# Kernel tuning notes

Measured on AMD Instinct MI355X. Metric: run time of the kernel, lower is better.

## Reference

```python
import jax, jax.numpy as jnp
import numpy as np

NEG_SLOPE = 0.2  # PyG GATConv default negative_slope
NUM_GRAPHS = 64
N, E, F_IN = 50000, 800000, 128


def _gat(x, src, dst, W, a_s, a_d, b, concat):
    # PyG GATConv: h = x W (per head); e_ij = leaky_relu(a_s.h_j + a_d.h_i);
    # softmax over incoming edges of each dst node; out_i = sum_j alpha_ij h_j
    n = x.shape[0]
    H, C = a_s.shape
    h = (x @ W).reshape(n, H, C)                     # [N,H,C]
    es = jnp.einsum('nhc,hc->nh', h, a_s)            # [N,H]
    ed = jnp.einsum('nhc,hc->nh', h, a_d)
    e = jax.nn.leaky_relu(es[src] + ed[dst], NEG_SLOPE)   # [E,H]
    m = jax.ops.segment_max(e, dst, num_segments=n)       # per-dst max (stable softmax)
    ex = jnp.exp(e - m[dst])
    den = jax.ops.segment_sum(ex, dst, num_segments=n)
    alpha = ex / den[dst]                                 # [E,H]
    out = jax.ops.segment_sum(h[src] * alpha[:, :, None], dst, num_segments=n)  # [N,H,C]
    if concat:
        return out.reshape(n, H * C) + b
    return out.mean(axis=1) + b


def setup_inputs() -> dict:
    key = jax.random.key(0)
    ks = jax.random.split(key, 10)
    x = jax.random.normal(ks[0], (N, F_IN), jnp.float32)
    edge_index = jax.random.randint(ks[1], (2, E), 0, N, dtype=jnp.int64)
    batch = jnp.sort(jax.random.randint(ks[2], (N,), 0, NUM_GRAPHS, dtype=jnp.int64))
    s1 = 1.0 / np.sqrt(F_IN)
    s2 = 1.0 / np.sqrt(256)
    return {
        'x': x,
        'edge_index': edge_index,
        'batch': batch,
        'W1': jax.random.normal(ks[3], (F_IN, 256), jnp.float32) * s1,
        'a_src1': jax.random.normal(ks[4], (4, 64), jnp.float32) * s2,
        'a_dst1': jax.random.normal(ks[5], (4, 64), jnp.float32) * s2,
        'b1': jnp.zeros((256,), jnp.float32),
        'W2': jax.random.normal(ks[6], (256, 128), jnp.float32) * s2,
        'a_src2': jax.random.normal(ks[7], (1, 128), jnp.float32) * (1.0 / np.sqrt(128)),
        'a_dst2': jax.random.normal(ks[8], (1, 128), jnp.float32) * (1.0 / np.sqrt(128)),
        'b2': jnp.zeros((128,), jnp.float32),
        'fc_w': jax.random.normal(ks[9], (128, 10), jnp.float32) * (1.0 / np.sqrt(128)),
        'fc_b': jnp.zeros((10,), jnp.float32),
    }


def reference(x, edge_index, batch, W1, a_src1, a_dst1, b1, W2, a_src2, a_dst2, b2, fc_w, fc_b):
    n = x.shape[0]
    loop = jnp.arange(n, dtype=edge_index.dtype)  # PyG add_self_loops=True
    src = jnp.concatenate([edge_index[0], loop])
    dst = jnp.concatenate([edge_index[1], loop])
    h = jax.nn.elu(_gat(x, src, dst, W1, a_src1, a_dst1, b1, True))   # dropout: eval mode -> identity
    h = jax.nn.elu(_gat(h, src, dst, W2, a_src2, a_dst2, b2, False))
    pooled = jax.ops.segment_sum(h, batch, num_segments=NUM_GRAPHS)
    cnt = jax.ops.segment_sum(jnp.ones((n,), h.dtype), batch, num_segments=NUM_GRAPHS)
    pooled = pooled / jnp.maximum(cnt, 1.0)[:, None]
    logits = pooled @ fc_w + fc_b
    return jax.nn.log_softmax(logits, axis=1)
```

## Files before the change

kernel.cpp:

```cpp
#include <hip/hip_runtime.h>
#include <math.h>

#define N_NODES 50000
#define N_PAD   50048
#define N_EDGES 800000
#define E_TOT   (N_EDGES + N_NODES)
#define NG 64
#define POOL_CHUNK 64
#define CAP 48
#define GEMM1_BLOCKS 3128
#define FILL_BLOCKS  3321
#define PH1_INTERLEAVE (2 * GEMM1_BLOCKS)
#define PH1_TOTAL (GEMM1_BLOCKS + FILL_BLOCKS)

typedef short short8 __attribute__((ext_vector_type(8)));
typedef float floatx4 __attribute__((ext_vector_type(4)));
typedef float floatx2 __attribute__((ext_vector_type(2)));

__device__ inline short f2bf(float f) {
    union { float f; unsigned u; } v; v.f = f;
    unsigned r = v.u + 0x7fff + ((v.u >> 16) & 1);
    return (short)(r >> 16);
}
__device__ inline float bf2f(short s) {
    union { float f; unsigned u; } v;
    v.u = ((unsigned)(unsigned short)s) << 16;
    return v.f;
}

__device__ inline unsigned f2fp8(float f) {
    union { float f; unsigned u; } v; v.f = f;
    unsigned s = v.u & 0x80000000u;
    unsigned au = v.u & 0x7fffffffu;
    if (au > 0x43E00000u) au = 0x43E00000u;
    unsigned r = au + 0x7ffffu + ((au >> 20) & 1);
    int e8 = (int)(r >> 23) - 120;
    unsigned m3 = (r >> 20) & 7;
    unsigned code;
    if (e8 <= 0) code = 0;
    else if (e8 > 15) code = 0x7e;
    else code = ((unsigned)e8 << 3) | m3;
    return (s >> 24) | code;
}

__device__ inline float leaky_exp(float t) {
    t = t > 0.f ? t : 0.2f * t;
    return __expf(t);
}


__global__ __launch_bounds__(256) void phase1_kernel(const float* __restrict__ x,
                                                     const float* __restrict__ W1,
                                                     const float* __restrict__ a_s,
                                                     const float* __restrict__ a_d,
                                                     const int* __restrict__ ei,
                                                     int* __restrict__ deg,
                                                     unsigned short* __restrict__ col,
                                                     unsigned char* __restrict__ C8,
                                                     float* __restrict__ es,
                                                     float* __restrict__ ed,
                                                     const float* __restrict__ W2,
                                                     const float* __restrict__ as2,
                                                     const float* __restrict__ ad2,
                                                     float* __restrict__ ws2,
                                                     float* __restrict__ wd2) {
    __shared__ short bs[64][136];
    int bid = blockIdx.x;
    int tid = threadIdx.x;

    if (bid == PH1_TOTAL) {
        int k = tid;
        float s = 0.f, d = 0.f;
        for (int c = 0; c < 128; c++) {
            float w = W2[k * 128 + c];
            s += w * as2[c];
            d += w * ad2[c];
        }
        ws2[k] = s;
        wd2[k] = d;
        return;
    }

    int gb, fb;
    if (bid < PH1_INTERLEAVE) {
        if (bid & 1) { fb = bid >> 1; gb = -1; }
        else         { gb = bid >> 1; fb = -1; }
    } else {
        fb = bid - GEMM1_BLOCKS; gb = -1;
    }

    if (fb >= 0) {
        int t = fb * 256 + tid;
        int s, d;
        if (t < N_EDGES) {
            s = ei[t];
            d = ei[N_EDGES + t];
        } else if (t < E_TOT) {
            s = d = t - N_EDGES;
        } else {
            return;
        }
        int slot = atomicAdd(&deg[d], 1);
        if (slot < CAP) col[d * CAP + slot] = (unsigned short)s;
        return;
    }

    const int K = 128, N = 256;
    int head = gb & 3;
    int bx = gb >> 2;
    int c0 = head * 64;

    int tc = tid & 63;
    int tk0 = (tid >> 6) * 32;
    for (int k = tk0; k < tk0 + 32; k++)
        bs[tc][k] = f2bf(W1[k * 256 + c0 + tc]);
    __syncthreads();

    int wid = tid >> 6;
    int lane = tid & 63;
    int m0 = bx * 64 + wid * 16;
    int mr = lane & 15;
    int quad = lane >> 4;
    int kq = quad << 3;
    int arow = m0 + mr; if (arow > N_NODES - 1) arow = N_NODES - 1;
    const float* aptr = x + (size_t)arow * K + kq;
    floatx4 acc[4] = {{0.f,0.f,0.f,0.f},{0.f,0.f,0.f,0.f},{0.f,0.f,0.f,0.f},{0.f,0.f,0.f,0.f}};
    for (int k0 = 0; k0 < K; k0 += 32) {
        float4 f0 = *(const float4*)(aptr + k0);
        float4 f1 = *(const float4*)(aptr + k0 + 4);
        short8 a;
        a[0] = f2bf(f0.x); a[1] = f2bf(f0.y); a[2] = f2bf(f0.z); a[3] = f2bf(f0.w);
        a[4] = f2bf(f1.x); a[5] = f2bf(f1.y); a[6] = f2bf(f1.z); a[7] = f2bf(f1.w);
#pragma unroll
        for (int t = 0; t < 4; t++) {
            short8 b = *(const short8*)&bs[t * 16 + mr][kq + k0];
            acc[t] = __builtin_amdgcn_mfma_f32_16x16x32_bf16(a, b, acc[t], 0, 0, 0);
        }
    }
    float asv[4], adv[4];
#pragma unroll
    for (int t = 0; t < 4; t++) {
        asv[t] = a_s[c0 + t * 16 + mr];
        adv[t] = a_d[c0 + t * 16 + mr];
    }
    int orow = m0 + (quad << 2);
#pragma unroll
    for (int r = 0; r < 4; r++) {
        float ps = acc[0][r] * asv[0] + acc[1][r] * asv[1] + acc[2][r] * asv[2] + acc[3][r] * asv[3];
        float pd = acc[0][r] * adv[0] + acc[1][r] * adv[1] + acc[2][r] * adv[2] + acc[3][r] * adv[3];
#pragma unroll
        for (int off = 8; off >= 1; off >>= 1) {
            ps += __shfl_xor(ps, off);
            pd += __shfl_xor(pd, off);
        }
        if (mr == 0) {
            es[(orow + r) * 4 + head] = ps;
            ed[(orow + r) * 4 + head] = pd;
        }
    }
#pragma unroll
    for (int t = 0; t < 4; t++) {
        int ocol = c0 + t * 16 + mr;
#pragma unroll
        for (int r = 0; r < 4; r++) {
            C8[(size_t)(orow + r) * N + ocol] = (unsigned char)f2fp8(acc[t][r]);
        }
    }
}


__global__ __launch_bounds__(256) void gather1_kernel(const unsigned char* __restrict__ h8,
                                                      const int* __restrict__ deg,
                                                      const unsigned short* __restrict__ col,
                                                      const float* __restrict__ es,
                                                      const float* __restrict__ ed,
                                                      const float* __restrict__ bias,
                                                      const float* __restrict__ ws2,
                                                      const float* __restrict__ wd2,
                                                      short* __restrict__ out,
                                                      float* __restrict__ es2,
                                                      float* __restrict__ ed2) {
    __shared__ float wlds[4][CAP * 4];
    int tid = threadIdx.x;
    int wid = tid >> 6;
    int n = __builtin_amdgcn_readfirstlane(blockIdx.x * 4 + wid);
    int l = tid & 63;
    int hh = l >> 4;
    int cnt = deg[n]; cnt = cnt < CAP ? cnt : CAP;
    int cnt8 = (cnt + 7) & ~7;

    {
        int eA = l >> 2;
        int hA = l & 3;
        float edvA = ed[n * 4 + hA];
#pragma unroll
        for (int p = 0; p < 3; p++) {
            int e = p * 16 + eA;
            if (e < cnt8) {
                int s = col[n * CAP + e];
                float w = (e < cnt) ? leaky_exp(es[s * 4 + hA] + edvA) : 0.f;
                wlds[wid][e * 4 + hA] = w;
            }
        }
    }

    const unsigned int* cp = (const unsigned int*)(col + n * CAP);
    float ax = 0.f, ay = 0.f, az = 0.f, aw = 0.f, den = 0.f;
    for (int eb = 0; eb < cnt8; eb += 8) {
        unsigned int cw0 = cp[(eb >> 1) + 0];
        unsigned int cw1 = cp[(eb >> 1) + 1];
        unsigned int cw2 = cp[(eb >> 1) + 2];
        unsigned int cw3 = cp[(eb >> 1) + 3];
        int idx[8];
        idx[0] = cw0 & 0xffff; idx[1] = cw0 >> 16;
        idx[2] = cw1 & 0xffff; idx[3] = cw1 >> 16;
        idx[4] = cw2 & 0xffff; idx[5] = cw2 >> 16;
        idx[6] = cw3 & 0xffff; idx[7] = cw3 >> 16;
        float wv[8];
#pragma unroll
        for (int j = 0; j < 8; j++) wv[j] = wlds[wid][(eb + j) * 4 + hh];
        unsigned hv[8];
#pragma unroll
        for (int j = 0; j < 8; j++)
            hv[j] = *(const unsigned*)&h8[(size_t)idx[j] * 256 + l * 4];
#pragma unroll
        for (int j = 0; j < 8; j++) {
            floatx2 lo = __builtin_amdgcn_cvt_pk_f32_fp8(hv[j], false);
            floatx2 hi = __builtin_amdgcn_cvt_pk_f32_fp8(hv[j], true);
            den += wv[j];
            ax += wv[j] * lo[0];
            ay += wv[j] * lo[1];
            az += wv[j] * hi[0];
            aw += wv[j] * hi[1];
        }
    }
    float inv = 1.0f / den;
    float4 bb = *(const float4*)&bias[l * 4];
    float o0 = ax * inv + bb.x;
    float o1 = ay * inv + bb.y;
    float o2 = az * inv + bb.z;
    float o3 = aw * inv + bb.w;
    o0 = o0 > 0.f ? o0 : __expf(o0) - 1.f;
    o1 = o1 > 0.f ? o1 : __expf(o1) - 1.f;
    o2 = o2 > 0.f ? o2 : __expf(o2) - 1.f;
    o3 = o3 > 0.f ? o3 : __expf(o3) - 1.f;
    short4 ob;
    ob.x = f2bf(o0); ob.y = f2bf(o1); ob.z = f2bf(o2); ob.w = f2bf(o3);
    *(short4*)&out[(size_t)n * 256 + l * 4] = ob;

    float4 s4 = *(const float4*)&ws2[l * 4];
    float4 d4 = *(const float4*)&wd2[l * 4];
    float ps = o0 * s4.x + o1 * s4.y + o2 * s4.z + o3 * s4.w;
    float pd = o0 * d4.x + o1 * d4.y + o2 * d4.z + o3 * d4.w;
#pragma unroll
    for (int off = 32; off >= 1; off >>= 1) {
        ps += __shfl_xor(ps, off);
        pd += __shfl_xor(pd, off);
    }
    if (l == 0) {
        es2[n] = ps;
        ed2[n] = pd;
    }
}


__global__ __launch_bounds__(256) void gemm2_kernel(const short* __restrict__ A,
                                                    const float* __restrict__ W2,
                                                    unsigned char* __restrict__ C8) {
    __shared__ short bs[64][264];
    const int K = 256, N = 128;
    int tid = threadIdx.x;
    int by = blockIdx.y;
    int c0 = by * 64;

    int tc = tid & 63;
    int tk0 = (tid >> 6) * 64;
    for (int k = tk0; k < tk0 + 64; k++)
        bs[tc][k] = f2bf(W2[k * 128 + c0 + tc]);
    __syncthreads();

    int wid = tid >> 6;
    int lane = tid & 63;
    int m0 = blockIdx.x * 64 + wid * 16;
    int mr = lane & 15;
    int quad = lane >> 4;
    int kq = quad << 3;
    const short* arow = A + (size_t)(m0 + mr) * K + kq;
    floatx4 acc[4] = {{0.f,0.f,0.f,0.f},{0.f,0.f,0.f,0.f},{0.f,0.f,0.f,0.f},{0.f,0.f,0.f,0.f}};
    for (int k0 = 0; k0 < K; k0 += 32) {
        short8 a = *(const short8*)(arow + k0);
#pragma unroll
        for (int t = 0; t < 4; t++) {
            short8 b = *(const short8*)&bs[t * 16 + mr][kq + k0];
            acc[t] = __builtin_amdgcn_mfma_f32_16x16x32_bf16(a, b, acc[t], 0, 0, 0);
        }
    }
    int orow = m0 + (quad << 2);
#pragma unroll
    for (int t = 0; t < 4; t++) {
        int ocol = c0 + t * 16 + mr;
#pragma unroll
        for (int r = 0; r < 4; r++) {
            C8[(size_t)(orow + r) * N + ocol] = (unsigned char)f2fp8(acc[t][r]);
        }
    }
}


__global__ __launch_bounds__(256) void gather2_kernel(const unsigned char* __restrict__ h8,
                                                      const int* __restrict__ deg,
                                                      const unsigned short* __restrict__ col,
                                                      const float* __restrict__ es2,
                                                      const float* __restrict__ ed2,
                                                      const float* __restrict__ bias,
                                                      short* __restrict__ out) {
    __shared__ float wlds[4][CAP];
    int tid = threadIdx.x;
    int wid = tid >> 6;
    int n = __builtin_amdgcn_readfirstlane(blockIdx.x * 4 + wid);
    int l = tid & 63;
    int cnt = deg[n]; cnt = cnt < CAP ? cnt : CAP;
    int cnt8 = (cnt + 7) & ~7;

    {
        float edv = ed2[n];
        if (l < cnt8) {
            int s = col[n * CAP + l];
            float w = (l < cnt) ? leaky_exp(es2[s] + edv) : 0.f;
            wlds[wid][l] = w;
        }
    }

    const unsigned int* cp = (const unsigned int*)(col + n * CAP);
    float ax = 0.f, ay = 0.f, den = 0.f;
    for (int eb = 0; eb < cnt8; eb += 8) {
        unsigned int cw0 = cp[(eb >> 1) + 0];
        unsigned int cw1 = cp[(eb >> 1) + 1];
        unsigned int cw2 = cp[(eb >> 1) + 2];
        unsigned int cw3 = cp[(eb >> 1) + 3];
        int idx[8];
        idx[0] = cw0 & 0xffff; idx[1] = cw0 >> 16;
        idx[2] = cw1 & 0xffff; idx[3] = cw1 >> 16;
        idx[4] = cw2 & 0xffff; idx[5] = cw2 >> 16;
        idx[6] = cw3 & 0xffff; idx[7] = cw3 >> 16;
        float wv[8];
#pragma unroll
        for (int j = 0; j < 8; j++) wv[j] = wlds[wid][eb + j];
        unsigned hv[8];
#pragma unroll
        for (int j = 0; j < 8; j++)
            hv[j] = *(const unsigned short*)&h8[(size_t)idx[j] * 128 + l * 2];
#pragma unroll
        for (int j = 0; j < 8; j++) {
            floatx2 lo = __builtin_amdgcn_cvt_pk_f32_fp8(hv[j], false);
            den += wv[j];
            ax += wv[j] * lo[0];
            ay += wv[j] * lo[1];
        }
    }
    float inv = 1.0f / den;
    float2 bb = *(const float2*)&bias[l * 2];
    float o0 = ax * inv + bb.x;
    float o1 = ay * inv + bb.y;
    o0 = o0 > 0.f ? o0 : __expf(o0) - 1.f;
    o1 = o1 > 0.f ? o1 : __expf(o1) - 1.f;
    short2 ob;
    ob.x = f2bf(o0); ob.y = f2bf(o1);
    *(short2*)&out[(size_t)n * 128 + l * 2] = ob;
}


__global__ __launch_bounds__(128) void pool1_kernel(const short* __restrict__ h,
                                                    const int* __restrict__ batch,
                                                    float* __restrict__ pooled) {
    int c = threadIdx.x;
    int n0 = blockIdx.x * POOL_CHUNK;
    int n1 = n0 + POOL_CHUNK;
    if (n1 > N_NODES) n1 = N_NODES;
    if (n0 >= n1) return;
    float acc = 0.f;
    int g = batch[n0];
    for (int n = n0; n < n1; n++) {
        int bg = batch[n];
        if (bg != g) {
            atomicAdd(&pooled[g * 128 + c], acc);
            acc = 0.f;
            g = bg;
        }
        acc += bf2f(h[n * 128 + c]);
    }
    atomicAdd(&pooled[g * 128 + c], acc);
}


__global__ void fc_kernel(const float* __restrict__ pooled, const int* __restrict__ batch,
                          const float* __restrict__ fcw, const float* __restrict__ fcb,
                          float* __restrict__ out) {
    int g = threadIdx.x;
    if (g >= NG) return;
    int lo = 0, hi = N_NODES;
    while (lo < hi) {
        int mid = (lo + hi) >> 1;
        if (batch[mid] < g) lo = mid + 1; else hi = mid;
    }
    int start = lo;
    lo = start; hi = N_NODES;
    while (lo < hi) {
        int mid = (lo + hi) >> 1;
        if (batch[mid] <= g) lo = mid + 1; else hi = mid;
    }
    int cnt = lo - start;
    float inv = 1.0f / (float)(cnt > 0 ? cnt : 1);

    float lg[10];
#pragma unroll
    for (int j = 0; j < 10; j++) lg[j] = fcb[j];
    for (int k = 0; k < 128; k++) {
        float p = pooled[g * 128 + k] * inv;
#pragma unroll
        for (int j = 0; j < 10; j++) lg[j] += p * fcw[k * 10 + j];
    }
    float m = lg[0];
#pragma unroll
    for (int j = 1; j < 10; j++) m = fmaxf(m, lg[j]);
    float se = 0.f;
#pragma unroll
    for (int j = 0; j < 10; j++) se += __expf(lg[j] - m);
    float lse = m + __logf(se);
#pragma unroll
    for (int j = 0; j < 10; j++) out[g * 10 + j] = lg[j] - lse;
}


extern "C" void kernel_launch(void* const* d_in, const int* in_sizes, int n_in,
                              void* d_out, int out_size, void* d_ws, size_t ws_size,
                              hipStream_t stream) {
    const float* x     = (const float*)d_in[0];
    const int*   ei    = (const int*)d_in[1];
    const int*   batch = (const int*)d_in[2];
    const float* W1    = (const float*)d_in[3];
    const float* as1   = (const float*)d_in[4];
    const float* ad1   = (const float*)d_in[5];
    const float* b1    = (const float*)d_in[6];
    const float* W2    = (const float*)d_in[7];
    const float* as2   = (const float*)d_in[8];
    const float* ad2   = (const float*)d_in[9];
    const float* b2    = (const float*)d_in[10];
    const float* fcw   = (const float*)d_in[11];
    const float* fcb   = (const float*)d_in[12];
    float* out = (float*)d_out;

    char* ws = (char*)d_ws;
    size_t off = 0;
    auto alloc = [&](size_t bytes) -> void* {
        void* p = ws + off;
        off = (off + bytes + 255) & ~(size_t)255;
        return p;
    };
    int* deg             = (int*)alloc(N_NODES * 4);
    float* pooled        = (float*)alloc(NG * 128 * 4);
    unsigned short* col  = (unsigned short*)alloc((size_t)N_NODES * CAP * 2);
    float* es1           = (float*)alloc((size_t)N_PAD * 4 * 4);
    float* ed1           = (float*)alloc((size_t)N_PAD * 4 * 4);
    float* es2           = (float*)alloc((size_t)N_PAD * 4);
    float* ed2           = (float*)alloc((size_t)N_PAD * 4);
    float* ws2           = (float*)alloc(256 * 4);
    float* wd2           = (float*)alloc(256 * 4);
    unsigned char* h1    = (unsigned char*)alloc((size_t)N_PAD * 256);
    short* h1p           = (short*)alloc((size_t)N_PAD * 256 * 2);
    unsigned char* h2    = (unsigned char*)alloc((size_t)N_PAD * 128);
    short* h2p           = (short*)alloc((size_t)N_PAD * 128 * 2);

    size_t zbytes = 200192 + ((size_t)NG * 128 * 4) + (size_t)N_NODES * CAP * 2;
    hipMemsetAsync(deg, 0, zbytes, stream);

    int ngrid = N_NODES / 4;

    phase1_kernel<<<PH1_TOTAL + 1, 256, 0, stream>>>(x, W1, as1, ad1, ei, deg, col, h1, es1, ed1,
                                                     W2, as2, ad2, ws2, wd2);
    gather1_kernel<<<ngrid, 256, 0, stream>>>(h1, deg, col, es1, ed1, b1, ws2, wd2,
                                              h1p, es2, ed2);
    gemm2_kernel<<<dim3(N_PAD / 64, 2), 256, 0, stream>>>(h1p, W2, h2);
    gather2_kernel<<<ngrid, 256, 0, stream>>>(h2, deg, col, es2, ed2, b2, h2p);

    pool1_kernel<<<(N_NODES + POOL_CHUNK - 1) / POOL_CHUNK, 128, 0, stream>>>(h2p, batch, pooled);
    fc_kernel<<<1, 64, 0, stream>>>(pooled, batch, fcw, fcb, out);
}
```

Measured before the change: 252.0 us.

## Shard CSR degree counters across 8 sub-buckets and compact adjacency in gather1

The edge-fill pass now spreads the per-destination atomic counters and adjacency slots across 8 shards chosen by block ID. This is meant to reduce atomic contention on the same deg entry and spread the col writes. gather1 merges the shards into a compact per-node list held in LDS, then writes a consolidated col/degT for gather2 to reuse. Block role interleaving between GEMM and fill blocks is also changed. The cost is more zeroing, 8 extra degree loads per node in gather1, and per-shard caps of 18 that could drop edges for skewed degrees.

```diff
diff --git a/kernel.cpp b/kernel.cpp
--- a/kernel.cpp
+++ b/kernel.cpp
@@ -8,6 +8,8 @@
 #define NG 64
 #define POOL_CHUNK 64
 #define CAP 48
+#define NSH 8
+#define SCAP 18
 #define GEMM1_BLOCKS 3128
 #define FILL_BLOCKS  3321
 #define PH1_INTERLEAVE (2 * GEMM1_BLOCKS)
@@ -54,8 +56,8 @@
                                                      const float* __restrict__ a_s,
                                                      const float* __restrict__ a_d,
                                                      const int* __restrict__ ei,
-                                                     int* __restrict__ deg,
-                                                     unsigned short* __restrict__ col,
+                                                     int* __restrict__ deg_s,
+                                                     unsigned short* __restrict__ col_s,
                                                      unsigned char* __restrict__ C8,
                                                      float* __restrict__ es,
                                                      float* __restrict__ ed,
@@ -81,12 +83,13 @@
         return;
     }
 
-    int gb, fb;
+    int gb = -1, fb = -1;
     if (bid < PH1_INTERLEAVE) {
-        if (bid & 1) { fb = bid >> 1; gb = -1; }
-        else         { gb = bid >> 1; fb = -1; }
+        int role = (bid ^ (bid >> 3)) & 1;
+        int gi = (bid >> 3) * 4 + ((bid & 7) >> 1);
+        if (role == 0) gb = gi; else fb = gi;
     } else {
-        fb = bid - GEMM1_BLOCKS; gb = -1;
+        fb = bid - GEMM1_BLOCKS;
     }
 
     if (fb >= 0) {
@@ -100,8 +103,9 @@
         } else {
             return;
         }
-        int slot = atomicAdd(&deg[d], 1);
-        if (slot < CAP) col[d * CAP + slot] = (unsigned short)s;
+        int sh = bid & 7;
+        int slot = atomicAdd(&deg_s[sh * N_NODES + d], 1);
+        if (slot < SCAP) col_s[((size_t)sh * N_NODES + d) * SCAP + slot] = (unsigned short)s;
         return;
     }
 
@@ -170,8 +174,8 @@
 
 
 __global__ __launch_bounds__(256) void gather1_kernel(const unsigned char* __restrict__ h8,
-                                                      const int* __restrict__ deg,
-                                                      const unsigned short* __restrict__ col,
+                                                      const int* __restrict__ deg_s,
+                                                      const unsigned short* __restrict__ col_s,
                                                       const float* __restrict__ es,
                                                       const float* __restrict__ ed,
                                                       const float* __restrict__ bias,
@@ -179,15 +183,47 @@
                                                       const float* __restrict__ wd2,
                                                       short* __restrict__ out,
                                                       float* __restrict__ es2,
-                                                      float* __restrict__ ed2) {
+                                                      float* __restrict__ ed2,
+                                                      int* __restrict__ degT,
+                                                      unsigned short* __restrict__ col) {
     __shared__ float wlds[4][CAP * 4];
+    __shared__ unsigned short ilds[4][CAP];
     int tid = threadIdx.x;
     int wid = tid >> 6;
     int n = __builtin_amdgcn_readfirstlane(blockIdx.x * 4 + wid);
     int l = tid & 63;
     int hh = l >> 4;
-    int cnt = deg[n]; cnt = cnt < CAP ? cnt : CAP;
+
+    int c0s = deg_s[0 * N_NODES + n]; if (c0s > SCAP) c0s = SCAP;
+    int c1s = deg_s[1 * N_NODES + n]; if (c1s > SCAP) c1s = SCAP;
+    int c2s = deg_s[2 * N_NODES + n]; if (c2s > SCAP) c2s = SCAP;
+    int c3s = deg_s[3 * N_NODES + n]; if (c3s > SCAP) c3s = SCAP;
+    int c4s = deg_s[4 * N_NODES + n]; if (c4s > SCAP) c4s = SCAP;
+    int c5s = deg_s[5 * N_NODES + n]; if (c5s > SCAP) c5s = SCAP;
+    int c6s = deg_s[6 * N_NODES + n]; if (c6s > SCAP) c6s = SCAP;
+    int c7s = deg_s[7 * N_NODES + n]; if (c7s > SCAP) c7s = SCAP;
+    int b1 = c0s, b2 = b1 + c1s, b3 = b2 + c2s, b4 = b3 + c3s;
+    int b5 = b4 + c4s, b6 = b5 + c5s, b7 = b6 + c6s;
+    int cnt = b7 + c7s; if (cnt > CAP) cnt = CAP;
     int cnt8 = (cnt + 7) & ~7;
+
+    unsigned short srcv = 0;
+    if (l < cnt) {
+        int base = 0, sh = 0;
+        if (l >= b1) { base = b1; sh = 1; }
+        if (l >= b2) { base = b2; sh = 2; }
+        if (l >= b3) { base = b3; sh = 3; }
+        if (l >= b4) { base = b4; sh = 4; }
+        if (l >= b5) { base = b5; sh = 5; }
+        if (l >= b6) { base = b6; sh = 6; }
+        if (l >= b7) { base = b7; sh = 7; }
+        srcv = col_s[((size_t)sh * N_NODES + n) * SCAP + (l - base)];
+    }
+    if (l < cnt8) {
+        ilds[wid][l] = srcv;
+        col[n * CAP + l] = srcv;
+    }
+    if (l == 0) degT[n] = cnt;
 
     {
         int eA = l >> 2;
@@ -197,25 +233,18 @@
         for (int p = 0; p < 3; p++) {
             int e = p * 16 + eA;
             if (e < cnt8) {
-                int s = col[n * CAP + e];
+                int s = ilds[wid][e];
                 float w = (e < cnt) ? leaky_exp(es[s * 4 + hA] + edvA) : 0.f;
                 wlds[wid][e * 4 + hA] = w;
             }
         }
     }
 
-    const unsigned int* cp = (const unsigned int*)(col + n * CAP);
     float ax = 0.f, ay = 0.f, az = 0.f, aw = 0.f, den = 0.f;
     for (int eb = 0; eb < cnt8; eb += 8) {
-        unsigned int cw0 = cp[(eb >> 1) + 0];
-        unsigned int cw1 = cp[(eb >> 1) + 1];
-        unsigned int cw2 = cp[(eb >> 1) + 2];
-        unsigned int cw3 = cp[(eb >> 1) + 3];
         int idx[8];
-        idx[0] = cw0 & 0xffff; idx[1] = cw0 >> 16;
-        idx[2] = cw1 & 0xffff; idx[3] = cw1 >> 16;
-        idx[4] = cw2 & 0xffff; idx[5] = cw2 >> 16;
-        idx[6] = cw3 & 0xffff; idx[7] = cw3 >> 16;
+#pragma unroll
+        for (int j = 0; j < 8; j++) idx[j] = ilds[wid][eb + j];
         float wv[8];
 #pragma unroll
         for (int j = 0; j < 8; j++) wv[j] = wlds[wid][(eb + j) * 4 + hh];
@@ -457,9 +486,11 @@
         off = (off + bytes + 255) & ~(size_t)255;
         return p;
     };
-    int* deg             = (int*)alloc(N_NODES * 4);
+    int* deg_s           = (int*)alloc((size_t)NSH * N_NODES * 4);
     float* pooled        = (float*)alloc(NG * 128 * 4);
+    int* degT            = (int*)alloc(N_NODES * 4);
     unsigned short* col  = (unsigned short*)alloc((size_t)N_NODES * CAP * 2);
+    unsigned short* col_s= (unsigned short*)alloc((size_t)NSH * N_NODES * SCAP * 2);
     float* es1           = (float*)alloc((size_t)N_PAD * 4 * 4);
     float* ed1           = (float*)alloc((size_t)N_PAD * 4 * 4);
     float* es2           = (float*)alloc((size_t)N_PAD * 4);
@@ -471,17 +502,17 @@
     unsigned char* h2    = (unsigned char*)alloc((size_t)N_PAD * 128);
     short* h2p           = (short*)alloc((size_t)N_PAD * 128 * 2);
 
-    size_t zbytes = 200192 + ((size_t)NG * 128 * 4) + (size_t)N_NODES * CAP * 2;
-    hipMemsetAsync(deg, 0, zbytes, stream);
+    size_t zbytes = (size_t)NSH * N_NODES * 4 + (size_t)NG * 128 * 4;
+    hipMemsetAsync(deg_s, 0, zbytes, stream);
 
     int ngrid = N_NODES / 4;
 
-    phase1_kernel<<<PH1_TOTAL + 1, 256, 0, stream>>>(x, W1, as1, ad1, ei, deg, col, h1, es1, ed1,
+    phase1_kernel<<<PH1_TOTAL + 1, 256, 0, stream>>>(x, W1, as1, ad1, ei, deg_s, col_s, h1, es1, ed1,
                                                      W2, as2, ad2, ws2, wd2);
-    gather1_kernel<<<ngrid, 256, 0, stream>>>(h1, deg, col, es1, ed1, b1, ws2, wd2,
-                                              h1p, es2, ed2);
+    gather1_kernel<<<ngrid, 256, 0, stream>>>(h1, deg_s, col_s, es1, ed1, b1, ws2, wd2,
+                                              h1p, es2, ed2, degT, col);
     gemm2_kernel<<<dim3(N_PAD / 64, 2), 256, 0, stream>>>(h1p, W2, h2);
-    gather2_kernel<<<ngrid, 256, 0, stream>>>(h2, deg, col, es2, ed2, b2, h2p);
+    gather2_kernel<<<ngrid, 256, 0, stream>>>(h2, degT, col, es2, ed2, b2, h2p);
 
     pool1_kernel<<<(N_NODES + POOL_CHUNK - 1) / POOL_CHUNK, 128, 0, stream>>>(h2p, batch, pooled);
     fc_kernel<<<1, 64, 0, stream>>>(pooled, batch, fcw, fcb, out);
```

Result: no change. 253.5 us (+0.6%).

## Build CSR via two-level bucket sort instead of global atomics

Applied to the files above, without the earlier changes.

Replaces the per-edge global atomicAdd scatter into the per-node column lists with a two-stage bucketed fill. Fill blocks first bin edges into 128 destination buckets using an LDS histogram and write packed (src,dlow) records. A new binfill kernel then assembles each bucket's column lists in LDS with shared atomics and writes them out coalesced, which also removes most of the memset. The gather kernel additionally stages column indices through LDS. The cost is an extra kernel launch and intermediate buffers, and records beyond the per-block bucket capacity are dropped, so heavily skewed inputs could lose edges.

```diff
diff --git a/kernel.cpp b/kernel.cpp
--- a/kernel.cpp
+++ b/kernel.cpp
@@ -8,9 +8,13 @@
 #define NG 64
 #define POOL_CHUNK 64
 #define CAP 48
+#define NBKT 128
+#define BNODES 391
+#define RCAP 48
+#define FILL_CHUNK 2048
 #define GEMM1_BLOCKS 3128
-#define FILL_BLOCKS  3321
-#define PH1_INTERLEAVE (2 * GEMM1_BLOCKS)
+#define FILL_BLOCKS  391
+#define PH1_DIAG (FILL_BLOCKS * 8)
 #define PH1_TOTAL (GEMM1_BLOCKS + FILL_BLOCKS)
 
 typedef short short8 __attribute__((ext_vector_type(8)));
@@ -54,8 +58,8 @@
                                                      const float* __restrict__ a_s,
                                                      const float* __restrict__ a_d,
                                                      const int* __restrict__ ei,
-                                                     int* __restrict__ deg,
-                                                     unsigned short* __restrict__ col,
+                                                     unsigned short* __restrict__ gcnt,
+                                                     unsigned* __restrict__ gb2,
                                                      unsigned char* __restrict__ C8,
                                                      float* __restrict__ es,
                                                      float* __restrict__ ed,
@@ -65,6 +69,7 @@
                                                      float* __restrict__ ws2,
                                                      float* __restrict__ wd2) {
     __shared__ short bs[64][136];
+    __shared__ int hist[NBKT];
     int bid = blockIdx.x;
     int tid = threadIdx.x;
 
@@ -81,27 +86,49 @@
         return;
     }
 
-    int gb, fb;
-    if (bid < PH1_INTERLEAVE) {
-        if (bid & 1) { fb = bid >> 1; gb = -1; }
-        else         { gb = bid >> 1; fb = -1; }
+    int gb = -1, fb = -1;
+    if (bid < PH1_DIAG) {
+        int g = bid >> 3, r = bid & 7;
+        if (r == (g & 7)) fb = g;
+        else gb = g * 7 + (r > (g & 7) ? r - 1 : r);
     } else {
-        fb = bid - GEMM1_BLOCKS; gb = -1;
+        gb = (PH1_DIAG - FILL_BLOCKS) + (bid - PH1_DIAG);
     }
 
     if (fb >= 0) {
-        int t = fb * 256 + tid;
-        int s, d;
-        if (t < N_EDGES) {
-            s = ei[t];
-            d = ei[N_EDGES + t];
-        } else if (t < E_TOT) {
-            s = d = t - N_EDGES;
-        } else {
-            return;
-        }
-        int slot = atomicAdd(&deg[d], 1);
-        if (slot < CAP) col[d * CAP + slot] = (unsigned short)s;
+        if (tid < NBKT) hist[tid] = 0;
+        __syncthreads();
+        unsigned meta[8], pay[8];
+        int e0 = fb * FILL_CHUNK;
+#pragma unroll
+        for (int j = 0; j < 8; j++) {
+            int t = e0 + j * 256 + tid;
+            if (t < N_EDGES) {
+                int s = ei[t];
+                int d = ei[N_EDGES + t];
+                unsigned bkt = (unsigned)d / 391u;
+                int dlow = d - (int)bkt * 391;
+                int pos = atomicAdd(&hist[bkt], 1);
+                meta[j] = (bkt << 16) | (unsigned)pos;
+                pay[j] = ((unsigned)s << 9) | (unsigned)dlow;
+            } else {
+                meta[j] = 0xffffffffu;
+            }
+        }
+        __syncthreads();
+        if (tid < NBKT) {
+            int c = hist[tid]; if (c > RCAP) c = RCAP;
+            gcnt[fb * NBKT + tid] = (unsigned short)c;
+        }
+#pragma unroll
+        for (int j = 0; j < 8; j++) {
+            if (meta[j] != 0xffffffffu) {
+                unsigned bkt = meta[j] >> 16;
+                unsigned pos = meta[j] & 0xffffu;
+                if (pos < RCAP)
+                    gb2[((size_t)bkt * FILL_BLOCKS + fb) * RCAP + pos] = pay[j];
+            }
+        }
         return;
     }
 
@@ -169,8 +196,51 @@
 }
 
 
+__global__ __launch_bounds__(256) void binfill_kernel(const unsigned* __restrict__ gb2,
+                                                      const unsigned short* __restrict__ gcnt,
+                                                      unsigned short* __restrict__ col,
+                                                      int* __restrict__ degT) {
+    __shared__ unsigned colL[BNODES * CAP / 2];
+    __shared__ int cnt[BNODES];
+    __shared__ unsigned short cl[FILL_BLOCKS + 1];
+    int b = blockIdx.x, tid = threadIdx.x;
+    for (int i = tid; i < BNODES * CAP / 2; i += 256) colL[i] = 0;
+    for (int i = tid; i < BNODES; i += 256) cnt[i] = 0;
+    for (int i = tid; i < FILL_BLOCKS; i += 256) cl[i] = gcnt[i * NBKT + b];
+    __syncthreads();
+    int nbase = b * BNODES;
+    for (int dl = tid; dl < BNODES; dl += 256) {
+        int nn = nbase + dl;
+        if (nn < N_NODES) {
+            cnt[dl] = 1;
+            ((unsigned short*)colL)[dl * CAP] = (unsigned short)nn;
+        }
+    }
+    __syncthreads();
+    const unsigned* src = gb2 + (size_t)b * FILL_BLOCKS * RCAP;
+    for (int i = tid; i < FILL_BLOCKS * RCAP; i += 256) {
+        int blk = i / RCAP;
+        int slot = i - blk * RCAP;
+        if (slot < (int)cl[blk]) {
+            unsigned p = src[i];
+            int dlow = p & 511;
+            int s = (int)(p >> 9);
+            int sp = atomicAdd(&cnt[dlow], 1);
+            if (sp < CAP) ((unsigned short*)colL)[dlow * CAP + sp] = (unsigned short)s;
+        }
+    }
+    __syncthreads();
+    unsigned* cb = (unsigned*)(col + (size_t)b * BNODES * CAP);
+    for (int i = tid; i < BNODES * CAP / 2; i += 256) cb[i] = colL[i];
+    for (int dl = tid; dl < BNODES; dl += 256) {
+        int nn = nbase + dl;
+        if (nn < N_NODES) degT[nn] = cnt[dl];
+    }
+}
+
+
 __global__ __launch_bounds__(256) void gather1_kernel(const unsigned char* __restrict__ h8,
-                                                      const int* __restrict__ deg,
+                                                      const int* __restrict__ degT,
                                                       const unsigned short* __restrict__ col,
                                                       const float* __restrict__ es,
                                                       const float* __restrict__ ed,
@@ -181,13 +251,16 @@
                                                       float* __restrict__ es2,
                                                       float* __restrict__ ed2) {
     __shared__ float wlds[4][CAP * 4];
+    __shared__ unsigned short ilds[4][CAP];
     int tid = threadIdx.x;
     int wid = tid >> 6;
     int n = __builtin_amdgcn_readfirstlane(blockIdx.x * 4 + wid);
     int l = tid & 63;
     int hh = l >> 4;
-    int cnt = deg[n]; cnt = cnt < CAP ? cnt : CAP;
+    int cnt = degT[n]; cnt = cnt < CAP ? cnt : CAP;
     int cnt8 = (cnt + 7) & ~7;
+
+    if (l < cnt8) ilds[wid][l] = col[n * CAP + l];
 
     {
         int eA = l >> 2;
@@ -197,25 +270,18 @@
         for (int p = 0; p < 3; p++) {
             int e = p * 16 + eA;
             if (e < cnt8) {
-                int s = col[n * CAP + e];
+                int s = ilds[wid][e];
                 float w = (e < cnt) ? leaky_exp(es[s * 4 + hA] + edvA) : 0.f;
                 wlds[wid][e * 4 + hA] = w;
             }
         }
     }
 
-    const unsigned int* cp = (const unsigned int*)(col + n * CAP);
     float ax = 0.f, ay = 0.f, az = 0.f, aw = 0.f, den = 0.f;
     for (int eb = 0; eb < cnt8; eb += 8) {
-        unsigned int cw0 = cp[(eb >> 1) + 0];
-        unsigned int cw1 = cp[(eb >> 1) + 1];
-        unsigned int cw2 = cp[(eb >> 1) + 2];
-        unsigned int cw3 = cp[(eb >> 1) + 3];
         int idx[8];
-        idx[0] = cw0 & 0xffff; idx[1] = cw0 >> 16;
-        idx[2] = cw1 & 0xffff; idx[3] = cw1 >> 16;
-        idx[4] = cw2 & 0xffff; idx[5] = cw2 >> 16;
-        idx[6] = cw3 & 0xffff; idx[7] = cw3 >> 16;
+#pragma unroll
+        for (int j = 0; j < 8; j++) idx[j] = ilds[wid][eb + j];
         float wv[8];
 #pragma unroll
         for (int j = 0; j < 8; j++) wv[j] = wlds[wid][(eb + j) * 4 + hh];
@@ -457,9 +523,11 @@
         off = (off + bytes + 255) & ~(size_t)255;
         return p;
     };
-    int* deg             = (int*)alloc(N_NODES * 4);
     float* pooled        = (float*)alloc(NG * 128 * 4);
-    unsigned short* col  = (unsigned short*)alloc((size_t)N_NODES * CAP * 2);
+    int* degT            = (int*)alloc((size_t)N_PAD * 4);
+    unsigned short* col  = (unsigned short*)alloc((size_t)NBKT * BNODES * CAP * 2);
+    unsigned* gb2        = (unsigned*)alloc((size_t)NBKT * FILL_BLOCKS * RCAP * 4);
+    unsigned short* gcnt = (unsigned short*)alloc((size_t)FILL_BLOCKS * NBKT * 2);
     float* es1           = (float*)alloc((size_t)N_PAD * 4 * 4);
     float* ed1           = (float*)alloc((size_t)N_PAD * 4 * 4);
     float* es2           = (float*)alloc((size_t)N_PAD * 4);
@@ -471,17 +539,17 @@
     unsigned char* h2    = (unsigned char*)alloc((size_t)N_PAD * 128);
     short* h2p           = (short*)alloc((size_t)N_PAD * 128 * 2);
 
-    size_t zbytes = 200192 + ((size_t)NG * 128 * 4) + (size_t)N_NODES * CAP * 2;
-    hipMemsetAsync(deg, 0, zbytes, stream);
+    hipMemsetAsync(pooled, 0, (size_t)NG * 128 * 4, stream);
 
     int ngrid = N_NODES / 4;
 
-    phase1_kernel<<<PH1_TOTAL + 1, 256, 0, stream>>>(x, W1, as1, ad1, ei, deg, col, h1, es1, ed1,
+    phase1_kernel<<<PH1_TOTAL + 1, 256, 0, stream>>>(x, W1, as1, ad1, ei, gcnt, gb2, h1, es1, ed1,
                                                      W2, as2, ad2, ws2, wd2);
-    gather1_kernel<<<ngrid, 256, 0, stream>>>(h1, deg, col, es1, ed1, b1, ws2, wd2,
+    binfill_kernel<<<NBKT, 256, 0, stream>>>(gb2, gcnt, col, degT);
+    gather1_kernel<<<ngrid, 256, 0, stream>>>(h1, degT, col, es1, ed1, b1, ws2, wd2,
                                               h1p, es2, ed2);
     gemm2_kernel<<<dim3(N_PAD / 64, 2), 256, 0, stream>>>(h1p, W2, h2);
-    gather2_kernel<<<ngrid, 256, 0, stream>>>(h2, deg, col, es2, ed2, b2, h2p);
+    gather2_kernel<<<ngrid, 256, 0, stream>>>(h2, degT, col, es2, ed2, b2, h2p);
 
     pool1_kernel<<<(N_NODES + POOL_CHUNK - 1) / POOL_CHUNK, 128, 0, stream>>>(h2p, batch, pooled);
     fc_kernel<<<1, 64, 0, stream>>>(pooled, batch, fcw, fcb, out);
```

Measured after the change: 260.5 us. 1.03x slower.
